# Kernel tuning notes

Measured on AMD Instinct MI355X. Metric: run time of the kernel, lower is better.

The kernel has to match this reference:

```python
import jax, jax.numpy as jnp
import numpy as np

B, S, E, H, DQ = 8, 1024, 128, 8, 128  # batch, seq, embedding_dim, head_num, qkv_dim
HD = H * DQ  # 1024


def setup_inputs() -> dict:
    key = jax.random.key(0)
    ks = jax.random.split(key, 8)
    q = jax.random.normal(ks[0], (B, S, E), dtype=jnp.float32)
    k = jax.random.normal(ks[1], (B, S, E), dtype=jnp.float32)
    v = jax.random.normal(ks[2], (B, S, E), dtype=jnp.float32)
    mask = jnp.zeros((B, S), dtype=jnp.float32)  # rank2 ninf mask (additive)
    scale = 0.02
    Wq = jax.random.normal(ks[3], (HD, E), dtype=jnp.float32) * scale  # torch Linear weight [out,in]
    Wk = jax.random.normal(ks[4], (HD, E), dtype=jnp.float32) * scale
    Wv = jax.random.normal(ks[5], (HD, E), dtype=jnp.float32) * scale
    Wc = jax.random.normal(ks[6], (E, HD), dtype=jnp.float32) * scale
    bc = jax.random.normal(ks[7], (E,), dtype=jnp.float32) * scale
    return {"q": q, "k": k, "v": v, "mask": mask,
            "Wq": Wq, "Wk": Wk, "Wv": Wv, "Wc": Wc, "bc": bc}


def reference(q, k, v, mask, Wq, Wk, Wv, Wc, bc):
    batch, n, emb = q.shape
    hd = Wq.shape[0]
    # Faithful to source quirk: head_num recomputed as out_features // in_features
    head_num = hd // emb
    BIG = 1e9
    EPS = 1e-12

    def heads(x):  # [B, n, HD] -> [B, H, n, d]
        return x.reshape(batch, -1, head_num, hd // head_num).transpose(0, 2, 1, 3)

    qh = heads(q @ Wq.T)
    kh = heads(k @ Wk.T)
    vh = heads(v @ Wv.T)
    d = qh.shape[-1]

    score = jnp.einsum('bhnd,bhmd->bhnm', qh, kh) / jnp.sqrt(jnp.float32(d))
    score = score + mask[:, None, None, :]
    score = jnp.nan_to_num(score, nan=-BIG, posinf=BIG, neginf=-BIG)
    w = jax.nn.softmax(score, axis=-1)
    w = jnp.nan_to_num(w, nan=0.0, posinf=0.0, neginf=0.0)
    w = jnp.maximum(w, 0.0)
    row_sum = jnp.sum(w, axis=-1, keepdims=True)
    # zero-row fallback: replace fully-masked rows with tiny uniform weights
    w = jnp.where(row_sum <= 0.0, EPS, w)
    row_sum = jnp.sum(w, axis=-1, keepdims=True)
    w = w / (row_sum + EPS)

    out = jnp.einsum('bhnm,bhmd->bhnd', w, vh)  # [B,H,n,d]
    out_concat = out.transpose(0, 2, 1, 3).reshape(batch, n, hd)
    return out_concat @ Wc.T + bc
```

## Files before the change

### kernel.cpp

```cpp
#include <hip/hip_runtime.h>

typedef __bf16 bf16;
typedef __attribute__((ext_vector_type(8))) __bf16 bf16x8;
typedef __attribute__((ext_vector_type(4))) __bf16 bf16x4;
typedef __attribute__((ext_vector_type(4))) float f32x4;

constexpr int Bb = 8;
constexpr int Ss = 1024;
constexpr int Ee = 128;
constexpr int Hh = 8;
constexpr int Dd = 128;
constexpr int HD = 1024;

__device__ __forceinline__ void gl_lds16(const bf16* gp, bf16* lp) {
    __builtin_amdgcn_global_load_lds(
        (const __attribute__((address_space(1))) unsigned int*)gp,
        (__attribute__((address_space(3))) unsigned int*)lp, 16, 0, 0);
}

__global__ void k_cvt(const float* __restrict__ Wq, const float* __restrict__ Wk,
                      const float* __restrict__ Wv,
                      bf16* __restrict__ Wqb, bf16* __restrict__ Wkb, bf16* __restrict__ Wvb)
{
    int gid = blockIdx.x * 256 + threadIdx.x;
    const float* src; bf16* dst; int off; float s = 1.0f;
    if      (gid < 32768) { src = Wq; dst = Wqb; off = gid;         s = 0.12751741530603157f; }
    else if (gid < 65536) { src = Wk; dst = Wkb; off = gid - 32768; }
    else                  { src = Wv; dst = Wvb; off = gid - 65536; }
    float4 f = ((const float4*)src)[off];
    bf16x4 p;
    p[0] = (bf16)(f.x * s); p[1] = (bf16)(f.y * s);
    p[2] = (bf16)(f.z * s); p[3] = (bf16)(f.w * s);
    ((bf16x4*)dst)[off] = p;
}

__global__ __launch_bounds__(256, 2) void k_qkv(
    const float* __restrict__ qin, const float* __restrict__ kin, const float* __restrict__ vin,
    const bf16* __restrict__ Wqb, const bf16* __restrict__ Wkb, const bf16* __restrict__ Wvb,
    bf16* __restrict__ Qh, bf16* __restrict__ Kh, bf16* __restrict__ Vt)
{
    const int rb    = blockIdx.x;
    const int h     = blockIdx.y;
    const int which = blockIdx.z;
    const float* x = (which == 0) ? qin : (which == 1) ? kin : vin;
    const bf16*  W = (which == 0) ? Wqb : (which == 1) ? Wkb : Wvb;

    __shared__ bf16 Xs[128][136];
    __shared__ bf16 Ws[128][136];

    const int tid  = threadIdx.x;
    const int wv   = tid >> 6;
    const int lane = tid & 63;
    const int lo   = lane & 15;
    const int q4   = lane >> 4;

#pragma unroll
    for (int t = 0; t < 8; ++t) {
        int c = tid + t * 256;
        int row = c >> 4, c8 = (c & 15) << 3;
        const float* xp = &x[(rb * 128 + row) * Ee + c8];
        float4 f0 = *(const float4*)xp;
        float4 f1 = *(const float4*)(xp + 4);
        bf16x8 p;
        p[0] = (bf16)f0.x; p[1] = (bf16)f0.y; p[2] = (bf16)f0.z; p[3] = (bf16)f0.w;
        p[4] = (bf16)f1.x; p[5] = (bf16)f1.y; p[6] = (bf16)f1.z; p[7] = (bf16)f1.w;
        *(bf16x8*)&Xs[row][c8] = p;
        *(bf16x8*)&Ws[row][c8] = *(const bf16x8*)&W[(h * 128 + row) * Ee + c8];
    }
    __syncthreads();

    const bf16 (*Ap)[136] = (which == 2) ? Ws : Xs;
    const bf16 (*Bp)[136] = (which == 2) ? Xs : Ws;

    f32x4 acc[2][8];
#pragma unroll
    for (int i = 0; i < 2; ++i)
#pragma unroll
        for (int j = 0; j < 8; ++j) acc[i][j] = f32x4{0.f, 0.f, 0.f, 0.f};

#pragma unroll
    for (int kq = 0; kq < 4; ++kq) {
        bf16x8 a[2], b8[8];
#pragma unroll
        for (int ri = 0; ri < 2; ++ri)
            a[ri] = *(const bf16x8*)&Ap[wv * 32 + ri * 16 + lo][kq * 32 + q4 * 8];
#pragma unroll
        for (int cj = 0; cj < 8; ++cj)
            b8[cj] = *(const bf16x8*)&Bp[cj * 16 + lo][kq * 32 + q4 * 8];
#pragma unroll
        for (int ri = 0; ri < 2; ++ri)
#pragma unroll
            for (int cj = 0; cj < 8; ++cj)
                acc[ri][cj] = __builtin_amdgcn_mfma_f32_16x16x32_bf16(
                    a[ri], b8[cj], acc[ri][cj], 0, 0, 0);
    }

    const int bb = rb >> 3;
    const int s0 = (rb & 7) * 128;
    if (which < 2) {
        bf16* dst = ((which == 0) ? Qh : Kh) + (bb * Hh + h) * Ss * Dd;
#pragma unroll
        for (int ri = 0; ri < 2; ++ri)
#pragma unroll
            for (int cj = 0; cj < 8; ++cj)
#pragma unroll
                for (int r = 0; r < 4; ++r) {
                    int row = wv * 32 + ri * 16 + q4 * 4 + r;
                    int col = cj * 16 + lo;
                    dst[(s0 + row) * Dd + col] = (bf16)acc[ri][cj][r];
                }
    } else {
        bf16* dst = Vt + (bb * Hh + h) * Dd * Ss;
#pragma unroll
        for (int ri = 0; ri < 2; ++ri)
#pragma unroll
            for (int cj = 0; cj < 8; ++cj)
#pragma unroll
                for (int r = 0; r < 4; ++r) {
                    int row = wv * 32 + ri * 16 + q4 * 4 + r;
                    int col = cj * 16 + lo;
                    dst[row * Ss + s0 + col] = (bf16)acc[ri][cj][r];
                }
    }
}

__global__ __launch_bounds__(256, 2) void k_attn(
    const bf16* __restrict__ Qh, const bf16* __restrict__ Kh, const bf16* __restrict__ Vt,
    const float* __restrict__ mask, bf16* __restrict__ oc)
{
    const int bh = blockIdx.x;
    const int qt = blockIdx.y;
    const int b  = bh >> 3;
    const int h  = bh & 7;
    const int tid  = threadIdx.x;
    const int wv   = tid >> 6;
    const int lane = tid & 63;
    const int lo   = lane & 15;
    const int q4   = lane >> 4;

    __shared__ bf16 KsL[64 * 128];
    __shared__ bf16 VsL[128 * 64];
    __shared__ bf16 Ps[4][32][72];
    __shared__ float maskS[1024];

    const bf16* Qb = Qh + bh * Ss * Dd;
    const bf16* Kb = Kh + bh * Ss * Dd;
    const bf16* Vb = Vt + bh * Dd * Ss;

#pragma unroll
    for (int t = 0; t < 4; ++t)
        maskS[tid + t * 256] = mask[b * Ss + tid + t * 256] * 1.4426950408889634f;

    const int q0 = qt * 128 + wv * 32;
    bf16x8 qf[2][4];
#pragma unroll
    for (int ri = 0; ri < 2; ++ri)
#pragma unroll
        for (int kq = 0; kq < 4; ++kq)
            qf[ri][kq] = *(const bf16x8*)&Qb[(q0 + ri * 16 + lo) * Dd + kq * 32 + q4 * 8];

    f32x4 accO[2][8];
#pragma unroll
    for (int i = 0; i < 2; ++i)
#pragma unroll
        for (int j = 0; j < 8; ++j) accO[i][j] = f32x4{0.f, 0.f, 0.f, 0.f};
    float lsum[2][4];
#pragma unroll
    for (int i = 0; i < 2; ++i)
#pragma unroll
        for (int r = 0; r < 4; ++r) lsum[i][r] = 0.f;

    const int sw = lo & 7;

    for (int kt = 0; kt < 16; ++kt) {
        const int j0 = kt * 64;
#pragma unroll
        for (int t = 0; t < 4; ++t) {
            int i = wv * 4 + t;
            int row = i * 4 + (lane >> 4);
            int g = (lane & 15) ^ (row & 7);
            gl_lds16(Kb + (j0 + row) * Dd + g * 8, &KsL[i * 512]);
        }
#pragma unroll
        for (int t = 0; t < 4; ++t) {
            int i = wv * 4 + t;
            int row = i * 8 + (lane >> 3);
            int g = (lane & 7) ^ (row & 7);
            gl_lds16(Vb + row * Ss + j0 + g * 8, &VsL[i * 512]);
        }
        __syncthreads();

        f32x4 sc[2][4];
#pragma unroll
        for (int i = 0; i < 2; ++i)
#pragma unroll
            for (int j = 0; j < 4; ++j) sc[i][j] = f32x4{0.f, 0.f, 0.f, 0.f};
#pragma unroll
        for (int kq = 0; kq < 4; ++kq) {
            bf16x8 kf[4];
#pragma unroll
            for (int cj = 0; cj < 4; ++cj)
                kf[cj] = *(const bf16x8*)&KsL[(cj * 16 + lo) * 128 + (((kq << 2) + q4) ^ sw) * 8];
#pragma unroll
            for (int ri = 0; ri < 2; ++ri)
#pragma unroll
                for (int cj = 0; cj < 4; ++cj)
                    sc[ri][cj] = __builtin_amdgcn_mfma_f32_16x16x32_bf16(
                        qf[ri][kq], kf[cj], sc[ri][cj], 0, 0, 0);
        }

        float mv[4];
#pragma unroll
        for (int cj = 0; cj < 4; ++cj) mv[cj] = maskS[j0 + cj * 16 + lo];

#pragma unroll
        for (int ri = 0; ri < 2; ++ri) {
#pragma unroll
            for (int r = 0; r < 4; ++r) {
                float p[4];
#pragma unroll
                for (int cj = 0; cj < 4; ++cj) p[cj] = exp2f(sc[ri][cj][r] + mv[cj]);
                lsum[ri][r] += (p[0] + p[1]) + (p[2] + p[3]);
                const int prow = ri * 16 + q4 * 4 + r;
#pragma unroll
                for (int cj = 0; cj < 4; ++cj)
                    Ps[wv][prow][cj * 16 + lo] = (bf16)p[cj];
            }
        }

#pragma unroll
        for (int kq = 0; kq < 2; ++kq) {
            bf16x8 pf[2];
#pragma unroll
            for (int ri = 0; ri < 2; ++ri)
                pf[ri] = *(const bf16x8*)&Ps[wv][ri * 16 + lo][kq * 32 + q4 * 8];
#pragma unroll
            for (int cj = 0; cj < 8; ++cj) {
                bf16x8 vf = *(const bf16x8*)&VsL[(cj * 16 + lo) * 64 + (((kq << 2) + q4) ^ sw) * 8];
#pragma unroll
                for (int ri = 0; ri < 2; ++ri)
                    accO[ri][cj] = __builtin_amdgcn_mfma_f32_16x16x32_bf16(
                        pf[ri], vf, accO[ri][cj], 0, 0, 0);
            }
        }
        __syncthreads();
    }

#pragma unroll
    for (int ri = 0; ri < 2; ++ri)
#pragma unroll
        for (int r = 0; r < 4; ++r) {
            float s = lsum[ri][r];
#pragma unroll
            for (int off = 1; off < 16; off <<= 1)
                s += __shfl_xor(s, off, 64);
            float inv = 1.0f / (s + 1e-12f);
            int sg = q0 + ri * 16 + q4 * 4 + r;
            bf16* dst = oc + (b * Ss + sg) * HD + h * 128;
#pragma unroll
            for (int cj = 0; cj < 8; ++cj)
                dst[cj * 16 + lo] = (bf16)(accO[ri][cj][r] * inv);
        }
}

__global__ __launch_bounds__(256, 4) void k_proj(
    const bf16* __restrict__ oc, const float* __restrict__ Wc,
    const float* __restrict__ bc, float* __restrict__ out)
{
    const int mt   = blockIdx.x;
    const int tid  = threadIdx.x;
    const int wv   = tid >> 6;
    const int lane = tid & 63;
    const int lo   = lane & 15;
    const int q4   = lane >> 4;

    f32x4 acc[2];
    acc[0] = f32x4{0.f, 0.f, 0.f, 0.f};
    acc[1] = f32x4{0.f, 0.f, 0.f, 0.f};

    const bf16* arow = oc + (mt * 16 + lo) * HD + q4 * 8;

    for (int kc = 0; kc < 8; ++kc) {
        const int k0 = kc * 128;
        bf16x8 a[4];
#pragma unroll
        for (int kq = 0; kq < 4; ++kq)
            a[kq] = *(const bf16x8*)&arow[k0 + kq * 32];
#pragma unroll
        for (int cj = 0; cj < 2; ++cj) {
            const int n = wv * 32 + cj * 16 + lo;
#pragma unroll
            for (int kq = 0; kq < 4; ++kq) {
                const float* wp = &Wc[n * HD + k0 + kq * 32 + q4 * 8];
                float4 f0 = *(const float4*)wp;
                float4 f1 = *(const float4*)(wp + 4);
                bf16x8 bfr;
                bfr[0] = (bf16)f0.x; bfr[1] = (bf16)f0.y; bfr[2] = (bf16)f0.z; bfr[3] = (bf16)f0.w;
                bfr[4] = (bf16)f1.x; bfr[5] = (bf16)f1.y; bfr[6] = (bf16)f1.z; bfr[7] = (bf16)f1.w;
                acc[cj] = __builtin_amdgcn_mfma_f32_16x16x32_bf16(
                    a[kq], bfr, acc[cj], 0, 0, 0);
            }
        }
    }

#pragma unroll
    for (int cj = 0; cj < 2; ++cj) {
        int col = wv * 32 + cj * 16 + lo;
        float bias = bc[col];
#pragma unroll
        for (int r = 0; r < 4; ++r) {
            int row = mt * 16 + q4 * 4 + r;
            out[row * Ee + col] = acc[cj][r] + bias;
        }
    }
}

extern "C" void kernel_launch(void* const* d_in, const int* in_sizes, int n_in,
                              void* d_out, int out_size, void* d_ws, size_t ws_size,
                              hipStream_t stream)
{
    const float* q    = (const float*)d_in[0];
    const float* k    = (const float*)d_in[1];
    const float* v    = (const float*)d_in[2];
    const float* mask = (const float*)d_in[3];
    const float* Wq   = (const float*)d_in[4];
    const float* Wk   = (const float*)d_in[5];
    const float* Wv   = (const float*)d_in[6];
    const float* Wc   = (const float*)d_in[7];
    const float* bc   = (const float*)d_in[8];
    float* out = (float*)d_out;

    constexpr int NBH = Bb * Hh * Ss * Dd;
    bf16* Qh = (bf16*)d_ws;
    bf16* Kh = Qh + NBH;
    bf16* Vt = Kh + NBH;
    bf16* oc = Vt + NBH;
    bf16* Wqb = oc;
    bf16* Wkb = Wqb + HD * Ee;
    bf16* Wvb = Wkb + HD * Ee;

    k_cvt<<<dim3(384), 256, 0, stream>>>(Wq, Wk, Wv, Wqb, Wkb, Wvb);
    k_qkv<<<dim3(64, 8, 3), 256, 0, stream>>>(q, k, v, Wqb, Wkb, Wvb, Qh, Kh, Vt);
    k_attn<<<dim3(64, 8), 256, 0, stream>>>(Qh, Kh, Vt, mask, oc);
    k_proj<<<dim3(512), 256, 0, stream>>>(oc, Wc, bc, out);
}
```

Baseline: 180.8 us.

## Keep softmax probabilities in registers via transposed MFMA, drop LDS P buffer

Computes S^T = K·Q^T so each lane's MFMA output already matches the B-operand layout of the PV MFMA. To make that work, K rows are loaded into LDS in a permuted order. This removes the per-wave Ps shared-memory round trip, along with its stores, barrier-free reads and LDS footprint. The output is computed transposed and written with 4-wide bf16 stores, and launch bounds are raised to 3 blocks per CU to use the freed LDS. The risks are register pressure at the higher occupancy target and correctness of the row permutation.

Result: slower. 187.0 us (+3.4%).

```diff
diff --git a/kernel.cpp b/kernel.cpp
--- a/kernel.cpp
+++ b/kernel.cpp
@@ -124,7 +124,7 @@
     }
 }
 
-__global__ __launch_bounds__(256, 2) void k_attn(
+__global__ __launch_bounds__(256, 3) void k_attn(
     const bf16* __restrict__ Qh, const bf16* __restrict__ Kh, const bf16* __restrict__ Vt,
     const float* __restrict__ mask, bf16* __restrict__ oc)
 {
@@ -140,7 +140,6 @@
 
     __shared__ bf16 KsL[64 * 128];
     __shared__ bf16 VsL[128 * 64];
-    __shared__ bf16 Ps[4][32][72];
     __shared__ float maskS[1024];
 
     const bf16* Qb = Qh + bh * Ss * Dd;
@@ -154,21 +153,17 @@
     const int q0 = qt * 128 + wv * 32;
     bf16x8 qf[2][4];
 #pragma unroll
-    for (int ri = 0; ri < 2; ++ri)
+    for (int nt = 0; nt < 2; ++nt)
 #pragma unroll
         for (int kq = 0; kq < 4; ++kq)
-            qf[ri][kq] = *(const bf16x8*)&Qb[(q0 + ri * 16 + lo) * Dd + kq * 32 + q4 * 8];
-
-    f32x4 accO[2][8];
-#pragma unroll
-    for (int i = 0; i < 2; ++i)
-#pragma unroll
-        for (int j = 0; j < 8; ++j) accO[i][j] = f32x4{0.f, 0.f, 0.f, 0.f};
-    float lsum[2][4];
-#pragma unroll
-    for (int i = 0; i < 2; ++i)
-#pragma unroll
-        for (int r = 0; r < 4; ++r) lsum[i][r] = 0.f;
+            qf[nt][kq] = *(const bf16x8*)&Qb[(q0 + nt * 16 + lo) * Dd + kq * 32 + q4 * 8];
+
+    f32x4 accO[8][2];
+#pragma unroll
+    for (int dm = 0; dm < 8; ++dm)
+#pragma unroll
+        for (int nt = 0; nt < 2; ++nt) accO[dm][nt] = f32x4{0.f, 0.f, 0.f, 0.f};
+    float lsum[2] = {0.f, 0.f};
 
     const int sw = lo & 7;
 
@@ -178,8 +173,10 @@
         for (int t = 0; t < 4; ++t) {
             int i = wv * 4 + t;
             int row = i * 4 + (lane >> 4);
+            int grow = (row & 32) + (((row >> 2) & 3) << 3)
+                     + (((row >> 4) & 1) << 2) + (row & 3);
             int g = (lane & 15) ^ (row & 7);
-            gl_lds16(Kb + (j0 + row) * Dd + g * 8, &KsL[i * 512]);
+            gl_lds16(Kb + (j0 + grow) * Dd + g * 8, &KsL[i * 512]);
         }
 #pragma unroll
         for (int t = 0; t < 4; ++t) {
@@ -190,77 +187,76 @@
         }
         __syncthreads();
 
-        f32x4 sc[2][4];
-#pragma unroll
-        for (int i = 0; i < 2; ++i)
-#pragma unroll
-            for (int j = 0; j < 4; ++j) sc[i][j] = f32x4{0.f, 0.f, 0.f, 0.f};
+        f32x4 sc[4][2];
+#pragma unroll
+        for (int c = 0; c < 4; ++c)
+#pragma unroll
+            for (int nt = 0; nt < 2; ++nt) sc[c][nt] = f32x4{0.f, 0.f, 0.f, 0.f};
 #pragma unroll
         for (int kq = 0; kq < 4; ++kq) {
             bf16x8 kf[4];
 #pragma unroll
-            for (int cj = 0; cj < 4; ++cj)
-                kf[cj] = *(const bf16x8*)&KsL[(cj * 16 + lo) * 128 + (((kq << 2) + q4) ^ sw) * 8];
-#pragma unroll
-            for (int ri = 0; ri < 2; ++ri)
-#pragma unroll
-                for (int cj = 0; cj < 4; ++cj)
-                    sc[ri][cj] = __builtin_amdgcn_mfma_f32_16x16x32_bf16(
-                        qf[ri][kq], kf[cj], sc[ri][cj], 0, 0, 0);
-        }
-
-        float mv[4];
-#pragma unroll
-        for (int cj = 0; cj < 4; ++cj) mv[cj] = maskS[j0 + cj * 16 + lo];
-
-#pragma unroll
-        for (int ri = 0; ri < 2; ++ri) {
-#pragma unroll
-            for (int r = 0; r < 4; ++r) {
-                float p[4];
-#pragma unroll
-                for (int cj = 0; cj < 4; ++cj) p[cj] = exp2f(sc[ri][cj][r] + mv[cj]);
-                lsum[ri][r] += (p[0] + p[1]) + (p[2] + p[3]);
-                const int prow = ri * 16 + q4 * 4 + r;
-#pragma unroll
-                for (int cj = 0; cj < 4; ++cj)
-                    Ps[wv][prow][cj * 16 + lo] = (bf16)p[cj];
+            for (int c = 0; c < 4; ++c)
+                kf[c] = *(const bf16x8*)&KsL[(c * 16 + lo) * 128 + (((kq << 2) + q4) ^ sw) * 8];
+#pragma unroll
+            for (int c = 0; c < 4; ++c)
+#pragma unroll
+                for (int nt = 0; nt < 2; ++nt)
+                    sc[c][nt] = __builtin_amdgcn_mfma_f32_16x16x32_bf16(
+                        kf[c], qf[nt][kq], sc[c][nt], 0, 0, 0);
+        }
+
+        bf16x8 p8[2][2];
+#pragma unroll
+        for (int kb = 0; kb < 2; ++kb) {
+#pragma unroll
+            for (int t = 0; t < 2; ++t) {
+                const float4 mv = *(const float4*)&maskS[j0 + kb * 32 + q4 * 8 + t * 4];
+                const int c = kb * 2 + t;
+#pragma unroll
+                for (int nt = 0; nt < 2; ++nt) {
+                    float e0 = exp2f(sc[c][nt][0] + mv.x);
+                    float e1 = exp2f(sc[c][nt][1] + mv.y);
+                    float e2 = exp2f(sc[c][nt][2] + mv.z);
+                    float e3 = exp2f(sc[c][nt][3] + mv.w);
+                    lsum[nt] += (e0 + e1) + (e2 + e3);
+                    p8[kb][nt][t * 4 + 0] = (bf16)e0;
+                    p8[kb][nt][t * 4 + 1] = (bf16)e1;
+                    p8[kb][nt][t * 4 + 2] = (bf16)e2;
+                    p8[kb][nt][t * 4 + 3] = (bf16)e3;
+                }
             }
         }
 
 #pragma unroll
-        for (int kq = 0; kq < 2; ++kq) {
-            bf16x8 pf[2];
-#pragma unroll
-            for (int ri = 0; ri < 2; ++ri)
-                pf[ri] = *(const bf16x8*)&Ps[wv][ri * 16 + lo][kq * 32 + q4 * 8];
-#pragma unroll
-            for (int cj = 0; cj < 8; ++cj) {
-                bf16x8 vf = *(const bf16x8*)&VsL[(cj * 16 + lo) * 64 + (((kq << 2) + q4) ^ sw) * 8];
-#pragma unroll
-                for (int ri = 0; ri < 2; ++ri)
-                    accO[ri][cj] = __builtin_amdgcn_mfma_f32_16x16x32_bf16(
-                        pf[ri], vf, accO[ri][cj], 0, 0, 0);
+        for (int kb = 0; kb < 2; ++kb)
+#pragma unroll
+            for (int dm = 0; dm < 8; ++dm) {
+                bf16x8 vf = *(const bf16x8*)&VsL[(dm * 16 + lo) * 64 + (((kb << 2) + q4) ^ sw) * 8];
+#pragma unroll
+                for (int nt = 0; nt < 2; ++nt)
+                    accO[dm][nt] = __builtin_amdgcn_mfma_f32_16x16x32_bf16(
+                        vf, p8[kb][nt], accO[dm][nt], 0, 0, 0);
             }
-        }
         __syncthreads();
     }
 
 #pragma unroll
-    for (int ri = 0; ri < 2; ++ri)
-#pragma unroll
-        for (int r = 0; r < 4; ++r) {
-            float s = lsum[ri][r];
-#pragma unroll
-            for (int off = 1; off < 16; off <<= 1)
-                s += __shfl_xor(s, off, 64);
-            float inv = 1.0f / (s + 1e-12f);
-            int sg = q0 + ri * 16 + q4 * 4 + r;
-            bf16* dst = oc + (b * Ss + sg) * HD + h * 128;
-#pragma unroll
-            for (int cj = 0; cj < 8; ++cj)
-                dst[cj * 16 + lo] = (bf16)(accO[ri][cj][r] * inv);
-        }
+    for (int nt = 0; nt < 2; ++nt) {
+        float s = lsum[nt];
+        s += __shfl_xor(s, 16, 64);
+        s += __shfl_xor(s, 32, 64);
+        float inv = 1.0f / (s + 1e-12f);
+        int sg = q0 + nt * 16 + lo;
+        bf16* dst = oc + (b * Ss + sg) * HD + h * 128;
+#pragma unroll
+        for (int dm = 0; dm < 8; ++dm) {
+            bf16x4 o;
+#pragma unroll
+            for (int r = 0; r < 4; ++r) o[r] = (bf16)(accO[dm][nt][r] * inv);
+            *(bf16x4*)&dst[dm * 16 + q4 * 4] = o;
+        }
+    }
 }
 
 __global__ __launch_bounds__(256, 4) void k_proj(
```
